# Kernel tuning notes

Hardware: AMD Instinct MI355X
Metric: run time of the kernel (lower is better)

The kernel has to match this reference:

```python
import jax, jax.numpy as jnp
import numpy as np

HEADS = 8
DIM_HEAD = 64
IMG = 32            # image_size
K = 5               # kernel_size
DIL = 1             # dilation
SEQ_LEN = 1279
SCALE = DIM_HEAD ** -0.5
IMG_SEQ = IMG * IMG                 # 1024
TEXT_LEN = SEQ_LEN + 1 - IMG_SEQ    # 256
NEG = -np.finfo(np.float32).max


def _unfold(img, pad_value):
    """torch F.unfold equivalent. img: [B, C, H, W] -> [B, H*W, K*K, C].
    Kernel-position index j is fastest-varying (matches torch unfold ordering
    after rearrange 'b (d j) i -> b i j d')."""
    B, C, H, W = img.shape
    p = ((K - 1) * DIL + 1) // 2
    padded = jnp.pad(img, ((0, 0), (0, 0), (p, p), (p, p)), constant_values=pad_value)
    patches = [padded[:, :, i * DIL:i * DIL + H, j * DIL:j * DIL + W]
               for i in range(K) for j in range(K)]
    pt = jnp.stack(patches, axis=2)            # [B, C, K*K, H, W]
    return pt.reshape(B, C, K * K, H * W).transpose(0, 3, 2, 1)


def _split_heads(t, b):
    # [b, N, h*d] -> [(b h), N, d]  (b slow, h fast)
    N = t.shape[1]
    return t.reshape(b, N, HEADS, DIM_HEAD).transpose(0, 2, 1, 3).reshape(b * HEADS, N, DIM_HEAD)


def setup_inputs() -> dict:
    key = jax.random.key(0)
    k1, k2, k3, k4 = jax.random.split(key, 4)
    dim = 512
    inner = HEADS * DIM_HEAD
    x = jax.random.normal(k1, (4, 1279, dim), dtype=jnp.float32)
    mask = jnp.ones((4, TEXT_LEN), dtype=bool)
    W_qkv = jax.random.normal(k2, (dim, inner * 3), dtype=jnp.float32) * 0.02
    W_out = jax.random.normal(k3, (inner, dim), dtype=jnp.float32) * 0.02
    b_out = jax.random.normal(k4, (dim,), dtype=jnp.float32) * 0.02
    return {"x": x, "mask": mask, "W_qkv": W_qkv, "W_out": W_out, "b_out": b_out}


def reference(x, mask, W_qkv, W_out, b_out):
    b, n, dim = x.shape
    pad = SEQ_LEN - n + 1
    xp = jnp.pad(x, ((0, 0), (0, pad), (0, 0)))            # [b, SEQ_LEN+1, dim]
    mask = mask[:, :TEXT_LEN]

    qkv = xp @ W_qkv
    q, k, v = jnp.split(qkv, 3, axis=-1)
    q = _split_heads(q, b) * SCALE                          # [(bh), N, d]
    k = _split_heads(k, b)
    v = _split_heads(v, b)

    q_text, q_img = q[:, :-IMG_SEQ], q[:, -IMG_SEQ:]
    k_text, k_img = k[:, :-IMG_SEQ], k[:, -IMG_SEQ:]
    v_text, v_img = v[:, :-IMG_SEQ], v[:, -IMG_SEQ:]

    # ---- text-to-text causal attention ----
    dots_text = jnp.einsum('bid,bjd->bij', q_text, k_text)
    tl = TEXT_LEN
    text_causal = jnp.triu(jnp.ones((tl, tl), dtype=bool), 1)
    dots_text = jnp.where(text_causal[None], NEG, dots_text)
    attn_text = jax.nn.softmax(dots_text, axis=-1)
    out_text = jnp.einsum('bij,bjd->bid', attn_text, v_text)

    # ---- local-window image attention (unfold) ----
    bh = b * HEADS
    k_img2 = k_img.reshape(bh, IMG, IMG, DIM_HEAD).transpose(0, 3, 1, 2)
    v_img2 = v_img.reshape(bh, IMG, IMG, DIM_HEAD).transpose(0, 3, 1, 2)
    k_imgu = _unfold(k_img2, 0.0)                           # [(bh), IMG_SEQ, K*K, d]
    v_imgu = _unfold(v_img2, 0.0)

    dots_image = jnp.einsum('bid,bijd->bij', q_img, k_imgu)         # [(bh), IMG_SEQ, K*K]
    dots_i2t = jnp.einsum('bid,bjd->bij', q_img, k_text)            # [(bh), IMG_SEQ, tl]

    # causal mask over local window via unfolded position indices
    idx = jnp.arange(IMG_SEQ, dtype=jnp.float32).reshape(1, 1, IMG, IMG)
    k_idx = _unfold(idx, float(IMG_SEQ))[..., 0]            # [1, IMG_SEQ, K*K]
    q_idx = jnp.arange(IMG_SEQ, dtype=jnp.float32)[None, :, None]
    causal_mask = q_idx < k_idx                             # [1, IMG_SEQ, K*K]

    text_pad_mask = jnp.repeat(~mask, HEADS, axis=0)[:, None, :]    # [(bh), 1, tl]
    full_mask = jnp.concatenate([
        jnp.broadcast_to(text_pad_mask, (bh, IMG_SEQ, tl)),
        jnp.broadcast_to(causal_mask, (bh, IMG_SEQ, K * K)),
    ], axis=-1)

    dots = jnp.concatenate([dots_i2t, dots_image], axis=-1)
    dots = jnp.where(full_mask, NEG, dots)
    attn = jax.nn.softmax(dots, axis=-1)
    attn_i2t, attn_img = attn[..., :tl], attn[..., tl:]

    out_image = (jnp.einsum('bij,bijd->bid', attn_img, v_imgu)
                 + jnp.einsum('bij,bjd->bid', attn_i2t, v_text))

    # ---- merge and project ----
    out = jnp.concatenate([out_text, out_image], axis=1)    # [(bh), N, d]
    N = out.shape[1]
    out = out.reshape(b, HEADS, N, DIM_HEAD).transpose(0, 2, 1, 3).reshape(b, N, HEADS * DIM_HEAD)
    out = out @ W_out + b_out
    return out[:, :n]
```

## Files before the change

kernel.cpp:

```cpp
#include <hip/hip_runtime.h>
#include <hip/hip_bf16.h>
#include <math.h>

#define HEADS   8
#define DH      64
#define IMGW    32
#define KKER    5
#define SEQ     1280
#define NTOK    1279
#define TL      256
#define IMG_SEQ 1024
#define DIM     512
#define BATCH   4
#define BH      32
#define SCALE   0.125f
#define NEGB    (-1.0e30f)

#define WQN  (DIM * 3 * DIM)
#define WON  (DIM * DIM)
#define QKVN ((size_t)BH * SEQ * DH)
#define AON  ((size_t)BATCH * SEQ * DIM)

#define XPBLK   1280
#define WQTILES 768
#define WOTILES 256


typedef unsigned short u16;
typedef __attribute__((ext_vector_type(8))) short bf16x8;
typedef __attribute__((ext_vector_type(4))) float f32x4;

__device__ inline u16 f2b(float f) {
    unsigned int u = __float_as_uint(f);
    return (u16)((u + 0x7FFFu + ((u >> 16) & 1u)) >> 16);
}
__device__ inline unsigned pack2(float a, float b) {
    return (unsigned)f2b(a) | ((unsigned)f2b(b) << 16);
}

__device__ inline void ldsload16(const u16* g, u16* l) {
    __builtin_amdgcn_global_load_lds(
        (const __attribute__((address_space(1))) unsigned int*)g,
        (__attribute__((address_space(3))) unsigned int*)l, 16, 0, 0);
}

__device__ inline void lds_barrier() {
    asm volatile("s_waitcnt lgkmcnt(0)\n\ts_barrier" ::: "memory");
}

__global__ __launch_bounds__(256) void cvt_all(
    const float* __restrict__ x, const float* __restrict__ Wq,
    const float* __restrict__ Wo, u16* __restrict__ xbf,
    u16* __restrict__ WqT, u16* __restrict__ WoT)
{
    __shared__ u16 tile[32][33];
    const int b = blockIdx.x;
    if (b < XPBLK) {
        const int i = b * 256 + threadIdx.x;
        const int row = i >> 6;
        const int bb = row / SEQ, nn = row % SEQ;
        union { unsigned u[4]; bf16x8 v; } r;
        if (nn < NTOK) {
            const size_t j = ((size_t)(bb * NTOK + nn) * 128 + (i & 63) * 2);
            const float4 a = ((const float4*)x)[j];
            const float4 c = ((const float4*)x)[j + 1];
            r.u[0] = pack2(a.x, a.y); r.u[1] = pack2(a.z, a.w);
            r.u[2] = pack2(c.x, c.y); r.u[3] = pack2(c.z, c.w);
        } else {
            r.u[0] = r.u[1] = r.u[2] = r.u[3] = 0u;
        }
        ((bf16x8*)xbf)[i] = r.v;
        return;
    }
    int t = b - XPBLK;
    const float* src; u16* dst; int C;
    if (t < WQTILES) { src = Wq; dst = WqT; C = 3 * DIM; }
    else             { t -= WQTILES; src = Wo; dst = WoT; C = DIM; }
    const int tc = C / 32;
    const int tr0 = (t / tc) * 32, tc0 = (t % tc) * 32;
    const int ty = threadIdx.x >> 5, tx = threadIdx.x & 31;
    #pragma unroll
    for (int s = 0; s < 4; s++) {
        const int r = ty + 8 * s;
        tile[r][tx] = f2b(src[(size_t)(tr0 + r) * C + tc0 + tx]);
    }
    __syncthreads();
    #pragma unroll
    for (int s = 0; s < 4; s++) {
        const int c = ty + 8 * s;
        dst[(size_t)(tc0 + c) * DIM + tr0 + tx] = tile[tx][c];
    }
}

__global__ __launch_bounds__(256) void qkv_mfma6(
    const u16* __restrict__ xbf, const u16* __restrict__ WqT,
    u16* __restrict__ Qbf, u16* __restrict__ Ktl, u16* __restrict__ Vtl)
{
    __shared__ u16 pool[12288];
    u16* const buf0 = pool;
    u16* const buf1 = pool + 6144;
    const int tid  = threadIdx.x;
    const int lane = tid & 63, wave = tid >> 6;
    const int quad = lane >> 4, l16 = lane & 15;
    const int wm = (wave >> 1) * 32, wn = (wave & 1) * 64;
    const int m0 = blockIdx.y * 64, n0 = blockIdx.x * 128;

    const u16* ga  = xbf + (size_t)(m0 + (tid >> 2)) * DIM + (tid & 3) * 8;
    const u16* gb0 = WqT + (size_t)(n0 + (tid >> 2)) * DIM + (tid & 3) * 8;
    const u16* gb1 = WqT + (size_t)(n0 + 64 + (tid >> 2)) * DIM + (tid & 3) * 8;

    f32x4 acc[2][4];
    #pragma unroll
    for (int i = 0; i < 2; i++)
        #pragma unroll
        for (int j = 0; j < 4; j++) acc[i][j] = (f32x4){0.f, 0.f, 0.f, 0.f};

    auto stage = [&](u16* b, int k) {
        ldsload16(ga  + k, b + wave * 512);
        ldsload16(gb0 + k, b + 2048 + wave * 512);
        ldsload16(gb1 + k, b + 4096 + wave * 512);
    };
    auto comp = [&](const u16* b) {
        bf16x8 af_[2], bf_[4];
        #pragma unroll
        for (int i = 0; i < 2; i++)
            af_[i] = *(const bf16x8*)&b[(wm + i * 16 + l16) * 32 + quad * 8];
        #pragma unroll
        for (int j = 0; j < 4; j++)
            bf_[j] = *(const bf16x8*)&b[2048 + (wn + j * 16 + l16) * 32 + quad * 8];
        #pragma unroll
        for (int i = 0; i < 2; i++)
            #pragma unroll
            for (int j = 0; j < 4; j++)
                acc[i][j] = __builtin_amdgcn_mfma_f32_16x16x32_bf16(
                    af_[i], bf_[j], acc[i][j], 0, 0, 0);
    };

    stage(buf0, 0);
    __syncthreads();
    for (int k0 = 0; k0 < DIM; k0 += 64) {
        stage(buf1, k0 + 32);
        comp(buf0);
        __syncthreads();
        if (k0 + 64 < DIM) stage(buf0, k0 + 64);
        comp(buf1);
        __syncthreads();
    }

    const int which = n0 >> 9;
    const float scl = (which == 0) ? SCALE : 1.f;
    #pragma unroll
    for (int i = 0; i < 2; i++)
        #pragma unroll
        for (int r = 0; r < 4; r++)
            #pragma unroll
            for (int j = 0; j < 4; j++)
                pool[(wm + i * 16 + quad * 4 + r) * 144 + wn + j * 16 + l16] =
                    f2b(acc[i][j][r] * scl);
    __syncthreads();

    const int b_  = m0 / SEQ;
    const int nn0 = m0 % SEQ;
    if (which == 0) {
        #pragma unroll
        for (int s = 0; s < 4; s++) {
            const int c   = tid + 256 * s;
            const int row = c >> 4, c8 = (c & 15) * 8;
            const int col511 = (n0 + c8) & 511;
            const int h = col511 >> 6, d0 = col511 & 63;
            const int bhh = b_ * HEADS + h;
            const bf16x8 v = *(const bf16x8*)&pool[row * 144 + c8];
            *(bf16x8*)&Qbf[((size_t)bhh * SEQ + nn0 + row) * DH + d0] = v;
        }
    } else if (which == 1) {
        #pragma unroll
        for (int s = 0; s < 4; s++) {
            const int c   = tid + 256 * s;
            const int row = c >> 4, c8 = (c & 15) * 8;
            const int col511 = (n0 + c8) & 511;
            const int h = col511 >> 6, d0 = col511 & 63;
            const int bhh = b_ * HEADS + h;
            const int key = nn0 + row;
            const bf16x8 v = *(const bf16x8*)&pool[row * 144 + c8];
            *(bf16x8*)&Ktl[(size_t)bhh * 81920 +
                (size_t)((((key >> 4) * 2 + (d0 >> 5)) * 512) +
                         ((key & 15) + 16 * ((d0 >> 3) & 3)) * 8)] = v;
        }
    } else {
        #pragma unroll
        for (int s = 0; s < 4; s++) {
            const int c   = tid + 256 * s;
            const int col = c & 127, r8 = (c >> 7) * 8;
            const int col511 = (n0 + col) & 511;
            const int h = col511 >> 6, d = col511 & 63;
            const int bhh = b_ * HEADS + h;
            const int key0 = nn0 + r8;
            union { u16 u[8]; bf16x8 v; } w;
            #pragma unroll
            for (int k = 0; k < 8; k++)
                w.u[k] = pool[(r8 + k) * 144 + col];
            *(bf16x8*)&Vtl[(size_t)bhh * 81920 +
                (size_t)((((key0 >> 5) * 4 + (d >> 4)) * 512) +
                         ((d & 15) + 16 * ((r8 >> 3) & 3)) * 8)] = w.v;
        }
    }
}

__global__ __launch_bounds__(256, 4) void attn_fused(
    const u16* __restrict__ Qbf, const u16* __restrict__ Ktl,
    const u16* __restrict__ Vtl, u16* __restrict__ AObf)
{
    const int id = blockIdx.x;
    const int bh = (id & 7) | (((id >> 3) & 3) << 3);
    const int bx = id >> 5;
    const bool istext = bx < 8;
    const int r0 = bx - 8;
    const int qt0 = istext ? bx * 32 : r0 * 32;
    const int qrow0 = istext ? qt0 : TL + qt0;
    const int tid = threadIdx.x;
    const int lane = tid & 63, wave = tid >> 6;
    const int quad = lane >> 4, l16 = lane & 15;

    __shared__ float Opool[4][2176];
    __shared__ float msm[4][32];
    __shared__ float mss[4][32];

    const int krs = istext ? 0 : min(max(r0 - 2, 0), IMGW - 5);
    const int cbase = TL + krs * 32;
    const bool tactive = !istext || (2 * wave <= bx);
    const bool xtra = (!istext) && (wave == 0);

    u16* const Pw = (u16*)Opool[wave];

    bf16x8 af[2][2];
    #pragma unroll
    for (int i = 0; i < 2; i++) {
        const u16* qr = Qbf + ((size_t)bh * SEQ + qrow0 + i * 16 + l16) * DH;
        af[i][0] = *(const bf16x8*)(qr + quad * 8);
        af[i][1] = *(const bf16x8*)(qr + 32 + quad * 8);
    }

    const u16* kt = Ktl + (size_t)bh * 81920;

    f32x4 sacc[2][4], cacc[2][2], xacc[2][2];
    #pragma unroll
    for (int i = 0; i < 2; i++) {
        #pragma unroll
        for (int j = 0; j < 4; j++) sacc[i][j] = (f32x4){0.f, 0.f, 0.f, 0.f};
        #pragma unroll
        for (int s = 0; s < 2; s++) {
            cacc[i][s] = (f32x4){0.f, 0.f, 0.f, 0.f};
            xacc[i][s] = (f32x4){0.f, 0.f, 0.f, 0.f};
        }
    }

    if (tactive) {
        bf16x8 kf0[4], kf1[4];
        #pragma unroll
        for (int j = 0; j < 4; j++) {
            kf0[j] = *(const bf16x8*)&kt[(size_t)(((wave * 4 + j) * 2) * 512) + lane * 8];
            kf1[j] = *(const bf16x8*)&kt[(size_t)(((wave * 4 + j) * 2 + 1) * 512) + lane * 8];
        }
        #pragma unroll
        for (int j = 0; j < 4; j++)
            #pragma unroll
            for (int i = 0; i < 2; i++) {
                sacc[i][j] = __builtin_amdgcn_mfma_f32_16x16x32_bf16(af[i][0], kf0[j], sacc[i][j], 0, 0, 0);
                sacc[i][j] = __builtin_amdgcn_mfma_f32_16x16x32_bf16(af[i][1], kf1[j], sacc[i][j], 0, 0, 0);
            }
    }
    if (!istext) {
        const int cb16 = cbase >> 4;
        {
            bf16x8 cf0[2], cf1[2];
            #pragma unroll
            for (int s = 0; s < 2; s++) {
                const int blk = cb16 + 2 * wave + s;
                cf0[s] = *(const bf16x8*)&kt[(size_t)((blk * 2) * 512) + lane * 8];
                cf1[s] = *(const bf16x8*)&kt[(size_t)((blk * 2 + 1) * 512) + lane * 8];
            }
            #pragma unroll
            for (int s = 0; s < 2; s++)
                #pragma unroll
                for (int i = 0; i < 2; i++) {
                    cacc[i][s] = __builtin_amdgcn_mfma_f32_16x16x32_bf16(af[i][0], cf0[s], cacc[i][s], 0, 0, 0);
                    cacc[i][s] = __builtin_amdgcn_mfma_f32_16x16x32_bf16(af[i][1], cf1[s], cacc[i][s], 0, 0, 0);
                }
        }
        if (xtra) {
            bf16x8 cf0[2], cf1[2];
            #pragma unroll
            for (int s = 0; s < 2; s++) {
                const int blk = cb16 + 8 + s;
                cf0[s] = *(const bf16x8*)&kt[(size_t)((blk * 2) * 512) + lane * 8];
                cf1[s] = *(const bf16x8*)&kt[(size_t)((blk * 2 + 1) * 512) + lane * 8];
            }
            #pragma unroll
            for (int s = 0; s < 2; s++)
                #pragma unroll
                for (int i = 0; i < 2; i++) {
                    xacc[i][s] = __builtin_amdgcn_mfma_f32_16x16x32_bf16(af[i][0], cf0[s], xacc[i][s], 0, 0, 0);
                    xacc[i][s] = __builtin_amdgcn_mfma_f32_16x16x32_bf16(af[i][1], cf1[s], xacc[i][s], 0, 0, 0);
                }
        }
    }

    float m8[2][4];
    #pragma unroll
    for (int i = 0; i < 2; i++)
        #pragma unroll
        for (int r = 0; r < 4; r++) {
            const int q = i * 16 + quad * 4 + r;
            float m = NEGB;
            if (istext) {
                if (tactive) {
                    const int qg = qt0 + q;
                    #pragma unroll
                    for (int j = 0; j < 4; j++) {
                        const int key = wave * 64 + j * 16 + l16;
                        const float v = (key <= qg) ? sacc[i][j][r] : NEGB;
                        sacc[i][j][r] = v;
                        m = fmaxf(m, v);
                    }
                }
            } else {
                const int qi = qt0 + q;
                #pragma unroll
                for (int j = 0; j < 4; j++) m = fmaxf(m, sacc[i][j][r]);
                #pragma unroll
                for (int s = 0; s < 2; s++) {
                    const int t = 2 * wave + s;
                    const int kidx = krs * 32 + t * 16 + l16;
                    const int kr = kidx >> 5, kc = kidx & 31;
                    const bool valid = (abs(kr - r0) <= 2) && (abs(kc - q) <= 2)
                                       && (kidx <= qi);
                    const float v = valid ? cacc[i][s][r] : NEGB;
                    cacc[i][s][r] = v;
                    m = fmaxf(m, v);
                }
                if (xtra) {
                    #pragma unroll
                    for (int s = 0; s < 2; s++) {
                        const int t = 8 + s;
                        const int kidx = krs * 32 + t * 16 + l16;
                        const int kr = kidx >> 5, kc = kidx & 31;
                        const bool valid = (abs(kr - r0) <= 2) && (abs(kc - q) <= 2)
                                           && (kidx <= qi);
                        const float v = valid ? xacc[i][s][r] : NEGB;
                        xacc[i][s][r] = v;
                        m = fmaxf(m, v);
                    }
                }
            }
            m8[i][r] = m;
        }
    #pragma unroll
    for (int off = 1; off < 16; off <<= 1)
        #pragma unroll
        for (int i = 0; i < 2; i++)
            #pragma unroll
            for (int r = 0; r < 4; r++)
                m8[i][r] = fmaxf(m8[i][r], __shfl_xor(m8[i][r], off));

    float s8[2][4];
    #pragma unroll
    for (int i = 0; i < 2; i++)
        #pragma unroll
        for (int r = 0; r < 4; r++) {
            const int q = i * 16 + quad * 4 + r;
            const float mr = m8[i][r];
            float s = 0.f;
            if (tactive) {
                #pragma unroll
                for (int j = 0; j < 4; j++) {
                    const float p = __expf(sacc[i][j][r] - mr);
                    Pw[q * 136 + j * 16 + l16] = f2b(p);
                    s += p;
                }
            }
            if (!istext) {
                #pragma unroll
                for (int ss = 0; ss < 2; ss++) {
                    const float p = __expf(cacc[i][ss][r] - mr);
                    Pw[q * 136 + 64 + ss * 16 + l16] = f2b(p);
                    s += p;
                }
                if (xtra) {
                    #pragma unroll
                    for (int ss = 0; ss < 2; ss++) {
                        const float p = __expf(xacc[i][ss][r] - mr);
                        Pw[q * 136 + 96 + ss * 16 + l16] = f2b(p);
                        s += p;
                    }
                }
            }
            s8[i][r] = s;
        }
    #pragma unroll
    for (int off = 1; off < 16; off <<= 1)
        #pragma unroll
        for (int i = 0; i < 2; i++)
            #pragma unroll
            for (int r = 0; r < 4; r++)
                s8[i][r] += __shfl_xor(s8[i][r], off);
    if (l16 == 0)
        #pragma unroll
        for (int i = 0; i < 2; i++)
            #pragma unroll
            for (int r = 0; r < 4; r++) {
                const int q = i * 16 + quad * 4 + r;
                msm[wave][q] = m8[i][r];
                mss[wave][q] = s8[i][r];
            }
    asm volatile("s_waitcnt lgkmcnt(0)" ::: "memory");

    bool cact[4];
    int ck[4];
    ck[0] = wave * 64; ck[1] = wave * 64 + 32;
    ck[2] = cbase + wave * 32; ck[3] = cbase + 128;
    if (istext) {
        cact[0] = tactive; cact[1] = (2 * wave + 1 <= bx);
        cact[2] = false;   cact[3] = false;
    } else {
        cact[0] = cact[1] = cact[2] = true; cact[3] = (wave == 0);
    }

    const u16* vt = Vtl + (size_t)bh * 81920;
    f32x4 o2[2][4];
    #pragma unroll
    for (int i = 0; i < 2; i++)
        #pragma unroll
        for (int j = 0; j < 4; j++) o2[i][j] = (f32x4){0.f, 0.f, 0.f, 0.f};

    #pragma unroll
    for (int c = 0; c < 4; c++) {
        if (cact[c]) {
            const bf16x8 av0 = *(const bf16x8*)&Pw[l16 * 136 + c * 32 + quad * 8];
            const bf16x8 av1 = *(const bf16x8*)&Pw[(16 + l16) * 136 + c * 32 + quad * 8];
            const int kcb = (ck[c] >> 5) * 4;
            bf16x8 bv[4];
            #pragma unroll
            for (int j = 0; j < 4; j++)
                bv[j] = *(const bf16x8*)&vt[(size_t)((kcb + j) * 512) + lane * 8];
            #pragma unroll
            for (int j = 0; j < 4; j++) {
                o2[0][j] = __builtin_amdgcn_mfma_f32_16x16x32_bf16(av0, bv[j], o2[0][j], 0, 0, 0);
                o2[1][j] = __builtin_amdgcn_mfma_f32_16x16x32_bf16(av1, bv[j], o2[1][j], 0, 0, 0);
            }
        }
    }

    #pragma unroll
    for (int i = 0; i < 2; i++)
        #pragma unroll
        for (int j = 0; j < 4; j++)
            #pragma unroll
            for (int r = 0; r < 4; r++)
                Opool[wave][(i * 16 + quad * 4 + r) * 68 + j * 16 + l16] = o2[i][j][r];

    lds_barrier();

    const int qq = tid >> 3, d8 = (tid & 7) * 8;
    const float mm = fmaxf(fmaxf(msm[0][qq], msm[1][qq]),
                           fmaxf(msm[2][qq], msm[3][qq]));
    float wgt[4];
    float den = 0.f;
    #pragma unroll
    for (int w = 0; w < 4; w++) {
        wgt[w] = __expf(msm[w][qq] - mm);
        den += mss[w][qq] * wgt[w];
    }
    float o[8];
    #pragma unroll
    for (int e = 0; e < 8; e++) o[e] = 0.f;
    #pragma unroll
    for (int w = 0; w < 4; w++) {
        const float* Ow = &Opool[w][qq * 68 + d8];
        #pragma unroll
        for (int e = 0; e < 8; e++) o[e] += Ow[e] * wgt[w];
    }
    const float inv = 1.f / den;
    union { u16 u[8]; bf16x8 v; } pk;
    #pragma unroll
    for (int e = 0; e < 8; e++) pk.u[e] = f2b(o[e] * inv);
    const int b_ = bh >> 3, h = bh & 7;
    *(bf16x8*)&AObf[((size_t)b_ * SEQ + qrow0 + qq) * DIM + h * DH + d8] = pk.v;
}

__global__ __launch_bounds__(256) void proj_mfma6(
    const u16* __restrict__ AObf, const u16* __restrict__ WoT,
    const float* __restrict__ bias, float* __restrict__ out)
{
    __shared__ u16 pool[10240];
    u16* const buf0 = pool;
    u16* const buf1 = pool + 5120;
    const int tid  = threadIdx.x;
    const int lane = tid & 63, wave = tid >> 6;
    const int quad = lane >> 4, l16 = lane & 15;
    const int wm = (wave >> 1) * 16, wn = (wave & 1) * 64;
    const int m0 = blockIdx.y * 32, n0 = blockIdx.x * 128;

    const u16* ga  = AObf + (size_t)(m0 + ((tid & 127) >> 2)) * DIM + (tid & 3) * 8;
    const u16* gb0 = WoT + (size_t)(n0 + (tid >> 2)) * DIM + (tid & 3) * 8;
    const u16* gb1 = WoT + (size_t)(n0 + 64 + (tid >> 2)) * DIM + (tid & 3) * 8;

    f32x4 acc[4];
    #pragma unroll
    for (int j = 0; j < 4; j++) acc[j] = (f32x4){0.f, 0.f, 0.f, 0.f};

    auto stage = [&](u16* b, int k) {
        if (wave < 2) ldsload16(ga + k, b + (wave & 1) * 512);
        ldsload16(gb0 + k, b + 1024 + wave * 512);
        ldsload16(gb1 + k, b + 3072 + wave * 512);
    };
    auto comp = [&](const u16* b) {
        const bf16x8 af = *(const bf16x8*)&b[(wm + l16) * 32 + quad * 8];
        bf16x8 bf_[4];
        #pragma unroll
        for (int j = 0; j < 4; j++)
            bf_[j] = *(const bf16x8*)&b[1024 + (wn + j * 16 + l16) * 32 + quad * 8];
        #pragma unroll
        for (int j = 0; j < 4; j++)
            acc[j] = __builtin_amdgcn_mfma_f32_16x16x32_bf16(af, bf_[j], acc[j], 0, 0, 0);
    };

    stage(buf0, 0);
    __syncthreads();
    for (int k0 = 0; k0 < DIM; k0 += 64) {
        stage(buf1, k0 + 32);
        comp(buf0);
        __syncthreads();
        if (k0 + 64 < DIM) stage(buf0, k0 + 64);
        comp(buf1);
        __syncthreads();
    }

    #pragma unroll
    for (int r = 0; r < 4; r++) {
        const int mm = m0 + wm + quad * 4 + r;
        const int bb = mm / SEQ, nn = mm % SEQ;
        if (nn >= NTOK) continue;
        const size_t mr = (size_t)(bb * NTOK + nn);
        #pragma unroll
        for (int j = 0; j < 4; j++) {
            const int ncol = n0 + wn + j * 16 + l16;
            out[mr * DIM + ncol] = acc[j][r] + bias[ncol];
        }
    }
}

extern "C" void kernel_launch(void* const* d_in, const int* in_sizes, int n_in,
                              void* d_out, int out_size, void* d_ws, size_t ws_size,
                              hipStream_t stream)
{
    const float* x    = (const float*)d_in[0];
    const float* Wqkv = (const float*)d_in[2];
    const float* Wout = (const float*)d_in[3];
    const float* bout = (const float*)d_in[4];
    float* out = (float*)d_out;

    u16* wsu  = (u16*)d_ws;
    u16* xbf  = wsu;
    u16* WqT  = xbf + AON;
    u16* WoT  = WqT + WQN;
    u16* Qbf  = WoT + WON;
    u16* Ktl  = Qbf + QKVN;
    u16* Vtl  = Ktl + QKVN;
    u16* AObf = Vtl + QKVN;

    cvt_all   <<<XPBLK + WQTILES + WOTILES, 256, 0, stream>>>(x, Wqkv, Wout, xbf, WqT, WoT);
    qkv_mfma6 <<<dim3(12, 80), 256, 0, stream>>>(xbf, WqT, Qbf, Ktl, Vtl);
    attn_fused<<<dim3(40 * BH), 256, 0, stream>>>(Qbf, Ktl, Vtl, AObf);
    proj_mfma6<<<dim3(4, 160), 256, 0, stream>>>(AObf, WoT, bout, out);
}
```

Baseline: 117.9 us.

## Remap GEMM blocks for XCD locality and pipeline LDS loads with explicit waitcnts

Both the QKV and output projection GEMMs now use a 1D grid whose block index is remapped so that consecutive blocks on each of the 8 XCDs share nearby tiles, which should improve L2 reuse. The K loop is fully unrolled. It keeps two async global-to-LDS stages in flight, using explicit vmcnt waits and raw s_barrier in place of __syncthreads, so loads overlap the MFMA work. The hand-tuned vmcnt counts depend on how many loads each wave issues per stage, which makes the code fragile if the stage function changes.

Result: no change. 116.6 us (-1.2%).

```diff
diff --git a/kernel.cpp b/kernel.cpp
--- a/kernel.cpp
+++ b/kernel.cpp
@@ -103,7 +103,10 @@
     const int lane = tid & 63, wave = tid >> 6;
     const int quad = lane >> 4, l16 = lane & 15;
     const int wm = (wave >> 1) * 32, wn = (wave & 1) * 64;
-    const int m0 = blockIdx.y * 64, n0 = blockIdx.x * 128;
+
+    const int id  = blockIdx.x;
+    const int nid = (id & 7) * 120 + (id >> 3);
+    const int m0 = (nid / 12) * 64, n0 = (nid % 12) * 128;
 
     const u16* ga  = xbf + (size_t)(m0 + (tid >> 2)) * DIM + (tid & 3) * 8;
     const u16* gb0 = WqT + (size_t)(n0 + (tid >> 2)) * DIM + (tid & 3) * 8;
@@ -137,18 +140,22 @@
     };
 
     stage(buf0, 0);
-    __syncthreads();
-    for (int k0 = 0; k0 < DIM; k0 += 64) {
-        stage(buf1, k0 + 32);
-        comp(buf0);
-        __syncthreads();
-        if (k0 + 64 < DIM) stage(buf0, k0 + 64);
-        comp(buf1);
-        __syncthreads();
+    stage(buf1, 32);
+    #pragma unroll
+    for (int s = 0; s < 16; s++) {
+        if (s == 15) asm volatile("s_waitcnt vmcnt(0)" ::: "memory");
+        else         asm volatile("s_waitcnt vmcnt(3)" ::: "memory");
+        __builtin_amdgcn_s_barrier();
+        comp((s & 1) ? buf1 : buf0);
+        asm volatile("s_waitcnt lgkmcnt(0)" ::: "memory");
+        __builtin_amdgcn_sched_barrier(0);
+        __builtin_amdgcn_s_barrier();
+        if (s < 14) stage((s & 1) ? buf1 : buf0, 32 * (s + 2));
     }
 
     const int which = n0 >> 9;
     const float scl = (which == 0) ? SCALE : 1.f;
+    __syncthreads();
     #pragma unroll
     for (int i = 0; i < 2; i++)
         #pragma unroll
@@ -498,7 +505,10 @@
     const int lane = tid & 63, wave = tid >> 6;
     const int quad = lane >> 4, l16 = lane & 15;
     const int wm = (wave >> 1) * 16, wn = (wave & 1) * 64;
-    const int m0 = blockIdx.y * 32, n0 = blockIdx.x * 128;
+
+    const int id  = blockIdx.x;
+    const int nid = (id & 7) * 80 + (id >> 3);
+    const int m0 = (nid / 4) * 32, n0 = (nid % 4) * 128;
 
     const u16* ga  = AObf + (size_t)(m0 + ((tid & 127) >> 2)) * DIM + (tid & 3) * 8;
     const u16* gb0 = WoT + (size_t)(n0 + (tid >> 2)) * DIM + (tid & 3) * 8;
@@ -525,14 +535,18 @@
     };
 
     stage(buf0, 0);
-    __syncthreads();
-    for (int k0 = 0; k0 < DIM; k0 += 64) {
-        stage(buf1, k0 + 32);
-        comp(buf0);
-        __syncthreads();
-        if (k0 + 64 < DIM) stage(buf0, k0 + 64);
-        comp(buf1);
-        __syncthreads();
+    stage(buf1, 32);
+    #pragma unroll
+    for (int s = 0; s < 16; s++) {
+        if (s == 15)        asm volatile("s_waitcnt vmcnt(0)" ::: "memory");
+        else if (wave < 2)  asm volatile("s_waitcnt vmcnt(3)" ::: "memory");
+        else                asm volatile("s_waitcnt vmcnt(2)" ::: "memory");
+        __builtin_amdgcn_s_barrier();
+        comp((s & 1) ? buf1 : buf0);
+        asm volatile("s_waitcnt lgkmcnt(0)" ::: "memory");
+        __builtin_amdgcn_sched_barrier(0);
+        __builtin_amdgcn_s_barrier();
+        if (s < 14) stage((s & 1) ? buf1 : buf0, 32 * (s + 2));
     }
 
     #pragma unroll
@@ -569,7 +583,7 @@
     u16* AObf = Vtl + QKVN;
 
     cvt_all   <<<XPBLK + WQTILES + WOTILES, 256, 0, stream>>>(x, Wqkv, Wout, xbf, WqT, WoT);
-    qkv_mfma6 <<<dim3(12, 80), 256, 0, stream>>>(xbf, WqT, Qbf, Ktl, Vtl);
+    qkv_mfma6 <<<dim3(960), 256, 0, stream>>>(xbf, WqT, Qbf, Ktl, Vtl);
     attn_fused<<<dim3(40 * BH), 256, 0, stream>>>(Qbf, Ktl, Vtl, AObf);
-    proj_mfma6<<<dim3(4, 160), 256, 0, stream>>>(AObf, WoT, bout, out);
-}
+    proj_mfma6<<<dim3(640), 256, 0, stream>>>(AObf, WoT, bout, out);
+}
```
